# Optimization experiments

Measured on AMD Instinct MI355X. Metric: run time of the kernel, lower is better.

Reference implementation:

```python
import jax, jax.numpy as jnp
import numpy as np

DIM = 2048; H = 16; DK = 128; DV = 128; SEQ = 2048; KCONV = 4
KEY_DIM = H * DK; VAL_DIM = H * DV
EPS_L2 = 1e-6; EPS_RMS = 1e-6; SP_THRESH = 20.0


def setup_inputs() -> dict:
    key = jax.random.key(0)
    ks = jax.random.split(key, 20)
    f = jnp.float32
    def w(k, shape, scale):
        return jax.random.normal(k, shape, f) * scale
    s_in = DIM ** -0.5
    return {
        "x": jax.random.normal(ks[0], (1, SEQ, DIM), f),
        "ve": jax.random.normal(ks[1], (1, SEQ, H, DV), f),
        "sa_lambdas": jnp.array([0.7, 0.3], f),
        "Wq": w(ks[2], (DIM, KEY_DIM), s_in),
        "Wk": w(ks[3], (DIM, KEY_DIM), s_in),
        "Wv": w(ks[4], (DIM, VAL_DIM), s_in),
        "conv_q": w(ks[5], (KEY_DIM, KCONV), 0.5),
        "conv_k": w(ks[6], (KEY_DIM, KCONV), 0.5),
        "conv_v": w(ks[7], (VAL_DIM, KCONV), 0.5),
        "Wf1": w(ks[8], (DIM, DV), s_in),
        "Wf2": w(ks[9], (DV, KEY_DIM), DV ** -0.5),
        "Wb": w(ks[10], (DIM, H), s_in),
        "A_log": jnp.log(jax.random.uniform(ks[11], (H,), f, 1.0, 16.0)),
        "dt_bias": jnp.zeros((KEY_DIM,), f),
        "Wg1": w(ks[12], (DIM, DV), s_in),
        "Wg2": w(ks[13], (DV, VAL_DIM), DV ** -0.5),
        "bg2": jnp.zeros((VAL_DIM,), f),
        "norm_w": jnp.ones((DV,), f),
        "Wo": w(ks[14], (VAL_DIM, DIM), VAL_DIM ** -0.5),
    }


def _short_conv_silu(u, w):
    # u: [b, s, c], w: [c, K]; causal depthwise conv + silu
    s = u.shape[1]
    up = jnp.pad(u, ((0, 0), (w.shape[1] - 1, 0), (0, 0)))
    y = sum(up[:, i:i + s, :] * w[:, i] for i in range(w.shape[1]))
    return jax.nn.silu(y)


def _l2norm(t):
    return t * jax.lax.rsqrt(jnp.sum(t * t, axis=-1, keepdims=True) + EPS_L2)


def _forward(x, ve, sa_lambdas, Wq, Wk, Wv, conv_q, conv_k, conv_v,
             Wf1, Wf2, Wb, A_log, dt_bias, Wg1, Wg2, bg2, norm_w, Wo):
    b, s, _ = x.shape  # b == 1
    q = _short_conv_silu(x @ Wq, conv_q).reshape(b, s, H, DK)
    k = _short_conv_silu(x @ Wk, conv_k).reshape(b, s, H, DK)
    v = _short_conv_silu(x @ Wv, conv_v).reshape(b, s, H, DV)
    v = sa_lambdas[0] * v + sa_lambdas[1] * ve
    # KDA gate: per-(head, key-dim) log decay
    g = ((x @ Wf1) @ Wf2).reshape(b, s, H, DK) + dt_bias.reshape(H, DK)
    sp = jnp.where(g > SP_THRESH, g, jnp.log1p(jnp.exp(jnp.minimum(g, SP_THRESH))))
    glog = -jnp.exp(A_log)[None, None, :, None] * sp  # [b,s,h,dk]
    beta = jax.nn.sigmoid(x @ Wb)  # [b,s,h]
    # l2-normalize q,k; scale q by dk^-0.5 (chunk_kda default scale)
    qn = _l2norm(q) * (DK ** -0.5)
    kn = _l2norm(k)
    # gated delta-rule recurrence over time (b==1, squeeze batch)
    def step(S, inp):
        qt, kt, vt, gt, bt = inp  # [h,dk],[h,dk],[h,dv],[h,dk],[h]
        S = S * jnp.exp(gt)[..., None]  # per-key-channel decay
        pred = jnp.einsum('hk,hkv->hv', kt, S)
        vt_new = bt[:, None] * (vt - pred)
        S = S + kt[:, :, None] * vt_new[:, None, :]
        ot = jnp.einsum('hk,hkv->hv', qt, S)
        return S, ot
    S0 = jnp.zeros((H, DK, DV), x.dtype)
    _, o = jax.lax.scan(step, S0, (qn[0], kn[0], v[0], glog[0], beta[0]))
    o = o[None]  # [1,s,h,dv]
    # sigmoid-gated RMSNorm over head_v_dim
    gate = ((x @ Wg1) @ Wg2 + bg2).reshape(b, s, H, DV)
    var = jnp.mean(o * o, axis=-1, keepdims=True)
    o = o * jax.lax.rsqrt(var + EPS_RMS) * norm_w
    o = o * jax.nn.sigmoid(gate)
    return o.reshape(b, s, VAL_DIM) @ Wo  # [1,s,dim]


def reference(x, ve, sa_lambdas, Wq, Wk, Wv, conv_q, conv_k, conv_v,
              Wf1, Wf2, Wb, A_log, dt_bias, Wg1, Wg2, bg2, norm_w, Wo):
    return _forward(x, ve, sa_lambdas, Wq, Wk, Wv, conv_q, conv_k, conv_v,
                    Wf1, Wf2, Wb, A_log, dt_bias, Wg1, Wg2, bg2, norm_w, Wo)
```

## Files before the change

kernel.cpp:

```cpp
#include <hip/hip_runtime.h>
#include <hip/hip_bf16.h>
#include <stdint.h>
#include <stddef.h>

#define SEQL 2048
#define DIMSZ 2048
#define HN 16
#define DKD 128
#define DVD 128
#define QSCALE 0.08838834764831843f

typedef __attribute__((ext_vector_type(4))) float f32x4;
typedef __attribute__((ext_vector_type(2))) float f32x2;
typedef __attribute__((ext_vector_type(8))) short bf16x8;

__device__ __forceinline__ float sigmoid_f(float x) { return 1.f / (1.f + __expf(-x)); }
__device__ __forceinline__ float bf2f(short s) {
  union { float f; unsigned int u; } t; t.u = ((unsigned int)(unsigned short)s) << 16; return t.f;
}

#define BM 128
#define BN 128
#define BKK 64

__global__ __launch_bounds__(256) void gemm_bt(
    const __hip_bfloat16* __restrict__ A, const __hip_bfloat16* __restrict__ B,
    float* __restrict__ C, int M, int N, int lda, int ldb, int klen, int accum)
{
  __shared__ __hip_bfloat16 As[BM * BKK];
  __shared__ __hip_bfloat16 Bs[BN * BKK];
  const int tid = threadIdx.x;
  const int lane = tid & 63;
  const int w = tid >> 6;
  const int wm = w >> 1, wn = w & 1;
  const int m0 = blockIdx.y * BM, n0 = blockIdx.x * BN;
  const int l15 = lane & 15, l4 = lane >> 4;
  const int kbase = blockIdx.z * klen;

  f32x4 acc[4][4] = {};

  for (int k0 = kbase; k0 < kbase + klen; k0 += BKK) {
#pragma unroll
    for (int i = 0; i < 4; ++i) {
      const int c = (w * 4 + i) * 64 + lane;
      const int row = c >> 3;
      const int colb = (c & 7) * 8;
      __builtin_amdgcn_global_load_lds(
          (const __attribute__((address_space(1))) void*)(A + (size_t)(m0 + row) * lda + k0 + colb),
          (__attribute__((address_space(3))) void*)(As + (size_t)c * 8), 16, 0, 0);
      __builtin_amdgcn_global_load_lds(
          (const __attribute__((address_space(1))) void*)(B + (size_t)(n0 + row) * ldb + k0 + colb),
          (__attribute__((address_space(3))) void*)(Bs + (size_t)c * 8), 16, 0, 0);
    }
    __syncthreads();
#pragma unroll
    for (int kk = 0; kk < BKK; kk += 32) {
      bf16x8 af[4], bfv[4];
#pragma unroll
      for (int mi = 0; mi < 4; ++mi)
        af[mi] = *(const bf16x8*)(As + (wm * 64 + mi * 16 + l15) * BKK + kk + l4 * 8);
#pragma unroll
      for (int ni = 0; ni < 4; ++ni)
        bfv[ni] = *(const bf16x8*)(Bs + (wn * 64 + ni * 16 + l15) * BKK + kk + l4 * 8);
#pragma unroll
      for (int mi = 0; mi < 4; ++mi)
#pragma unroll
        for (int ni = 0; ni < 4; ++ni)
          acc[mi][ni] = __builtin_amdgcn_mfma_f32_16x16x32_bf16(af[mi], bfv[ni], acc[mi][ni], 0, 0, 0);
    }
    __syncthreads();
  }

  float* Cz = C + (size_t)blockIdx.z * M * N;
#pragma unroll
  for (int mi = 0; mi < 4; ++mi) {
#pragma unroll
    for (int ni = 0; ni < 4; ++ni) {
      const int row = m0 + wm * 64 + mi * 16 + l4 * 4;
      const int col = n0 + wn * 64 + ni * 16 + l15;
#pragma unroll
      for (int r = 0; r < 4; ++r) {
        size_t idx = (size_t)(row + r) * N + col;
        if (accum) Cz[idx] += acc[mi][ni][r];
        else Cz[idx] = acc[mi][ni][r];
      }
    }
  }
}

#define PHASE256(MQ, NQ, NEEDA, NEEDB)                                          \
  {                                                                             \
    if (NEEDA) {                                                                \
      _Pragma("unroll") for (int m2 = 0; m2 < 4; ++m2)                          \
      _Pragma("unroll") for (int ks = 0; ks < 2; ++ks) {                        \
        const int la = (MQ) * 128 + wm * 64 + m2 * 16 + l15;                    \
        const int kc = ks * 4 + l4;                                             \
        a[m2][ks] = *(const bf16x8*)(lds + cb + la * 64 + (kc ^ (la & 7)) * 8); \
      }                                                                         \
    }                                                                           \
    if (NEEDB) {                                                                \
      _Pragma("unroll") for (int n2 = 0; n2 < 2; ++n2)                          \
      _Pragma("unroll") for (int ks = 0; ks < 2; ++ks) {                        \
        const int lb = (NQ) * 128 + wn * 32 + n2 * 16 + l15;                    \
        const int kc = ks * 4 + l4;                                             \
        b[n2][ks] = *(const bf16x8*)(lds + cb + 16384 + lb * 64 + (kc ^ (lb & 7)) * 8); \
      }                                                                         \
    }                                                                           \
    __builtin_amdgcn_s_setprio(1);                                              \
    _Pragma("unroll") for (int m2 = 0; m2 < 4; ++m2)                            \
    _Pragma("unroll") for (int n2 = 0; n2 < 2; ++n2)                            \
    _Pragma("unroll") for (int ks = 0; ks < 2; ++ks)                            \
      acc[(MQ) * 4 + m2][(NQ) * 2 + n2] = __builtin_amdgcn_mfma_f32_16x16x32_bf16( \
          a[m2][ks], b[n2][ks], acc[(MQ) * 4 + m2][(NQ) * 2 + n2], 0, 0, 0);    \
    __builtin_amdgcn_s_setprio(0);                                              \
  }

__global__ __launch_bounds__(512, 2) void gemm_bt256(
    const __hip_bfloat16* __restrict__ A, const __hip_bfloat16* __restrict__ B,
    float* __restrict__ C, __hip_bfloat16* __restrict__ Cb,
    int M, int N, int lda, int ldb, int NT)
{
  __shared__ __hip_bfloat16 lds[65536];
  const int tid = threadIdx.x;
  const int w = tid >> 6, lane = tid & 63;
  const int wm = w >> 2, wn = w & 3;
  const int l15 = lane & 15, l4 = lane >> 4;
  const int m0 = blockIdx.y * 256, n0 = blockIdx.x * 256;

  f32x4 acc[8][4] = {};
  bf16x8 a[4][2], b[2][2];

  auto stage_half = [&](int which, int t1) {
    const int buf = t1 & 1;
    const int k0n = ((t1 < NT) ? t1 : 0) * 64;
    const int mat = which & 1;
    const int half = which >> 1;
#pragma unroll
    for (int i = 0; i < 2; ++i) {
      const int c = i * 512 + tid;
      const int l = half * 128 + (c >> 3);
      const int kcs = (c & 7) ^ (l & 7);
      const __hip_bfloat16* src;
      if (mat == 0) {
        const int grow = ((l >> 6) & 1) * 128 + (l >> 7) * 64 + (l & 63);
        src = A + (size_t)(m0 + grow) * lda + k0n + kcs * 8;
      } else {
        const int gcol = ((l >> 5) & 3) * 64 + (l >> 7) * 32 + (l & 31);
        src = B + (size_t)(n0 + gcol) * ldb + k0n + kcs * 8;
      }
      __builtin_amdgcn_global_load_lds(
          (const __attribute__((address_space(1))) void*)src,
          (__attribute__((address_space(3))) void*)(lds + (size_t)buf * 32768 + mat * 16384 + half * 8192 + (size_t)c * 8),
          16, 0, 0);
    }
  };

  stage_half(0, 0); stage_half(1, 0); stage_half(2, 0); stage_half(3, 0);

  for (int t = 0; t < NT; ++t) {
    const size_t cb = (size_t)(t & 1) * 32768;
    stage_half(0, t + 1);
    asm volatile("s_waitcnt vmcnt(6)" ::: "memory");
    __builtin_amdgcn_s_barrier();
    __builtin_amdgcn_sched_barrier(0);
    PHASE256(0, 0, 1, 1)
    __builtin_amdgcn_s_barrier();
    stage_half(1, t + 1);
    asm volatile("s_waitcnt vmcnt(4)" ::: "memory");
    __builtin_amdgcn_s_barrier();
    __builtin_amdgcn_sched_barrier(0);
    PHASE256(0, 1, 0, 1)
    __builtin_amdgcn_s_barrier();
    stage_half(2, t + 1);
    __builtin_amdgcn_s_barrier();
    __builtin_amdgcn_sched_barrier(0);
    PHASE256(1, 1, 1, 0)
    __builtin_amdgcn_s_barrier();
    stage_half(3, t + 1);
    __builtin_amdgcn_s_barrier();
    __builtin_amdgcn_sched_barrier(0);
    PHASE256(1, 0, 0, 1)
    __builtin_amdgcn_s_barrier();
  }
  asm volatile("s_waitcnt vmcnt(0)" ::: "memory");

  if (Cb) {
#pragma unroll
    for (int mi = 0; mi < 8; ++mi)
#pragma unroll
      for (int ni = 0; ni < 4; ++ni) {
        const int row = m0 + wm * 128 + mi * 16 + l4 * 4;
        const int col = n0 + wn * 64 + ni * 16 + l15;
#pragma unroll
        for (int r = 0; r < 4; ++r)
          Cb[(size_t)(row + r) * N + col] = __float2bfloat16(acc[mi][ni][r]);
      }
  } else {
#pragma unroll
    for (int mi = 0; mi < 8; ++mi)
#pragma unroll
      for (int ni = 0; ni < 4; ++ni) {
        const int row = m0 + wm * 128 + mi * 16 + l4 * 4;
        const int col = n0 + wn * 64 + ni * 16 + l15;
#pragma unroll
        for (int r = 0; r < 4; ++r)
          C[(size_t)(row + r) * N + col] = acc[mi][ni][r];
      }
  }
}

__global__ __launch_bounds__(256) void gemm_btsplit(
    const __hip_bfloat16* __restrict__ Ah, const __hip_bfloat16* __restrict__ Al,
    const __hip_bfloat16* __restrict__ Bh, const __hip_bfloat16* __restrict__ Bl,
    float* __restrict__ C, int M, int N, int lda, int ldb, int klen)
{
  __shared__ __hip_bfloat16 Ash[BM * BKK];
  __shared__ __hip_bfloat16 Asl[BM * BKK];
  __shared__ __hip_bfloat16 Bsh[BN * BKK];
  __shared__ __hip_bfloat16 Bsl[BN * BKK];
  const int tid = threadIdx.x;
  const int lane = tid & 63;
  const int w = tid >> 6;
  const int wm = w >> 1, wn = w & 1;
  const int m0 = blockIdx.y * BM, n0 = blockIdx.x * BN;
  const int l15 = lane & 15, l4 = lane >> 4;
  const int kbase = blockIdx.z * klen;

  f32x4 acc[4][4] = {};

  for (int k0 = kbase; k0 < kbase + klen; k0 += BKK) {
#pragma unroll
    for (int i = 0; i < 4; ++i) {
      const int c = (w * 4 + i) * 64 + lane;
      const int row = c >> 3;
      const int colb = (c & 7) * 8;
      const size_t go = (size_t)(m0 + row) * lda + k0 + colb;
      const size_t gn = (size_t)(n0 + row) * ldb + k0 + colb;
      __builtin_amdgcn_global_load_lds(
          (const __attribute__((address_space(1))) void*)(Ah + go),
          (__attribute__((address_space(3))) void*)(Ash + (size_t)c * 8), 16, 0, 0);
      __builtin_amdgcn_global_load_lds(
          (const __attribute__((address_space(1))) void*)(Al + go),
          (__attribute__((address_space(3))) void*)(Asl + (size_t)c * 8), 16, 0, 0);
      __builtin_amdgcn_global_load_lds(
          (const __attribute__((address_space(1))) void*)(Bh + gn),
          (__attribute__((address_space(3))) void*)(Bsh + (size_t)c * 8), 16, 0, 0);
      __builtin_amdgcn_global_load_lds(
          (const __attribute__((address_space(1))) void*)(Bl + gn),
          (__attribute__((address_space(3))) void*)(Bsl + (size_t)c * 8), 16, 0, 0);
    }
    __syncthreads();
#pragma unroll
    for (int kk = 0; kk < BKK; kk += 32) {
      bf16x8 afh[4], afl[4], bfh[4], bfl[4];
#pragma unroll
      for (int mi = 0; mi < 4; ++mi) {
        const int ao = (wm * 64 + mi * 16 + l15) * BKK + kk + l4 * 8;
        afh[mi] = *(const bf16x8*)(Ash + ao);
        afl[mi] = *(const bf16x8*)(Asl + ao);
      }
#pragma unroll
      for (int ni = 0; ni < 4; ++ni) {
        const int bo = (wn * 64 + ni * 16 + l15) * BKK + kk + l4 * 8;
        bfh[ni] = *(const bf16x8*)(Bsh + bo);
        bfl[ni] = *(const bf16x8*)(Bsl + bo);
      }
#pragma unroll
      for (int mi = 0; mi < 4; ++mi)
#pragma unroll
        for (int ni = 0; ni < 4; ++ni) {
          acc[mi][ni] = __builtin_amdgcn_mfma_f32_16x16x32_bf16(afh[mi], bfh[ni], acc[mi][ni], 0, 0, 0);
          acc[mi][ni] = __builtin_amdgcn_mfma_f32_16x16x32_bf16(afh[mi], bfl[ni], acc[mi][ni], 0, 0, 0);
          acc[mi][ni] = __builtin_amdgcn_mfma_f32_16x16x32_bf16(afl[mi], bfh[ni], acc[mi][ni], 0, 0, 0);
        }
    }
    __syncthreads();
  }

  float* Cz = C + (size_t)blockIdx.z * M * N;
#pragma unroll
  for (int mi = 0; mi < 4; ++mi) {
#pragma unroll
    for (int ni = 0; ni < 4; ++ni) {
      const int row = m0 + wm * 64 + mi * 16 + l4 * 4;
      const int col = n0 + wn * 64 + ni * 16 + l15;
#pragma unroll
      for (int r = 0; r < 4; ++r)
        Cz[(size_t)(row + r) * N + col] = acc[mi][ni][r];
    }
  }
}

__global__ __launch_bounds__(256) void transpose4_kernel(
    const float* __restrict__ Wq, const float* __restrict__ Wk,
    const float* __restrict__ Wv, const float* __restrict__ Wo,
    __hip_bfloat16* __restrict__ WqkvT, __hip_bfloat16* __restrict__ WoT)
{
  __shared__ float tile[32][33];
  const int z = blockIdx.z;
  const float* in = (z == 0) ? Wq : (z == 1) ? Wk : (z == 2) ? Wv : Wo;
  __hip_bfloat16* outT = (z < 3) ? (WqkvT + (size_t)z * 2048 * 2048) : WoT;
  const int c0 = blockIdx.x * 32, r0 = blockIdx.y * 32;
  const int tc = threadIdx.x & 31, tr = threadIdx.x >> 5;
#pragma unroll
  for (int i = 0; i < 4; ++i)
    tile[tr + i * 8][tc] = in[(size_t)(r0 + tr + i * 8) * 2048 + c0 + tc];
  __syncthreads();
#pragma unroll
  for (int i = 0; i < 4; ++i)
    outT[(size_t)(c0 + tr + i * 8) * 2048 + r0 + tc] = __float2bfloat16(tile[tc][tr + i * 8]);
}

__global__ __launch_bounds__(256) void transpose_fg1_kernel(
    const float* __restrict__ Wf1, const float* __restrict__ Wg1,
    __hip_bfloat16* __restrict__ hT, __hip_bfloat16* __restrict__ lT)
{
  __shared__ float tile[32][33];
  const int z = blockIdx.z;
  const float* in = z ? Wg1 : Wf1;
  const size_t base = (size_t)z * 128 * 2048;
  const int c0 = blockIdx.x * 32, r0 = blockIdx.y * 32;
  const int tc = threadIdx.x & 31, tr = threadIdx.x >> 5;
#pragma unroll
  for (int i = 0; i < 4; ++i)
    tile[tr + i * 8][tc] = in[(size_t)(r0 + tr + i * 8) * 128 + c0 + tc];
  __syncthreads();
#pragma unroll
  for (int i = 0; i < 4; ++i) {
    float val = tile[tc][tr + i * 8];
    __hip_bfloat16 h = __float2bfloat16(val);
    size_t oi = base + (size_t)(c0 + tr + i * 8) * 2048 + r0 + tc;
    hT[oi] = h;
    lT[oi] = z ? __float2bfloat16(0.f) : __float2bfloat16(val - __bfloat162float(h));
  }
}

__global__ __launch_bounds__(256) void transpose_f2g2_kernel(
    const float* __restrict__ Wf2, const float* __restrict__ Wg2,
    __hip_bfloat16* __restrict__ f2h, __hip_bfloat16* __restrict__ f2l,
    __hip_bfloat16* __restrict__ g2h)
{
  __shared__ float tile[32][33];
  const int z = blockIdx.z;
  const float* in = z ? Wg2 : Wf2;
  const int c0 = blockIdx.x * 32, r0 = blockIdx.y * 32;
  const int tc = threadIdx.x & 31, tr = threadIdx.x >> 5;
#pragma unroll
  for (int i = 0; i < 4; ++i)
    tile[tr + i * 8][tc] = in[(size_t)(r0 + tr + i * 8) * 2048 + c0 + tc];
  __syncthreads();
#pragma unroll
  for (int i = 0; i < 4; ++i) {
    float val = tile[tc][tr + i * 8];
    __hip_bfloat16 h = __float2bfloat16(val);
    size_t oi = (size_t)(c0 + tr + i * 8) * 128 + r0 + tc;
    if (z == 0) { f2h[oi] = h; f2l[oi] = __float2bfloat16(val - __bfloat162float(h)); }
    else g2h[oi] = h;
  }
}

__global__ __launch_bounds__(256) void cast_split_kernel(
    const float* __restrict__ in, __hip_bfloat16* __restrict__ hi,
    __hip_bfloat16* __restrict__ lo, int n4)
{
  int idx = blockIdx.x * 256 + threadIdx.x;
  if (idx >= n4) return;
  f32x4 v = *(const f32x4*)(in + (size_t)idx * 4);
  union { __hip_bfloat16 b[4]; unsigned long long u; } ph, pl;
#pragma unroll
  for (int j = 0; j < 4; ++j) {
    float f = v[j];
    __hip_bfloat16 hh = __float2bfloat16(f);
    ph.b[j] = hh;
    pl.b[j] = __float2bfloat16(f - __bfloat162float(hh));
  }
  *(unsigned long long*)((char*)hi + (size_t)idx * 8) = ph.u;
  if (lo) *(unsigned long long*)((char*)lo + (size_t)idx * 8) = pl.u;
}

__global__ __launch_bounds__(256) void reduce8_kernel(
    const float* __restrict__ part, __hip_bfloat16* __restrict__ hi,
    __hip_bfloat16* __restrict__ lo, int n4, size_t chunk)
{
  int idx = blockIdx.x * 256 + threadIdx.x;
  if (idx >= n4) return;
  f32x4 a = *(const f32x4*)(part + (size_t)idx * 4);
#pragma unroll
  for (int z = 1; z < 8; ++z) {
    f32x4 b = *(const f32x4*)(part + z * chunk + (size_t)idx * 4);
    a.x += b.x; a.y += b.y; a.z += b.z; a.w += b.w;
  }
  union { __hip_bfloat16 b[4]; unsigned long long u; } ph, pl;
#pragma unroll
  for (int j = 0; j < 4; ++j) {
    float f = a[j];
    __hip_bfloat16 hh = __float2bfloat16(f);
    ph.b[j] = hh;
    pl.b[j] = __float2bfloat16(f - __bfloat162float(hh));
  }
  *(unsigned long long*)((char*)hi + (size_t)idx * 8) = ph.u;
  if (lo) *(unsigned long long*)((char*)lo + (size_t)idx * 8) = pl.u;
}

__global__ __launch_bounds__(256) void beta_kernel(
    const float* __restrict__ x, const float* __restrict__ Wb, float* __restrict__ betaT)
{
  int idx = blockIdx.x * 256 + threadIdx.x;
  int s = idx >> 4, h = idx & 15;
  const float* xr = x + (size_t)s * DIMSZ;
  float acc = 0.f;
  for (int d = 0; d < DIMSZ; d += 4) {
    f32x4 xv = *(const f32x4*)(xr + d);
    acc = fmaf(xv.x, Wb[(size_t)(d + 0) * HN + h], acc);
    acc = fmaf(xv.y, Wb[(size_t)(d + 1) * HN + h], acc);
    acc = fmaf(xv.z, Wb[(size_t)(d + 2) * HN + h], acc);
    acc = fmaf(xv.w, Wb[(size_t)(d + 3) * HN + h], acc);
  }
  betaT[(size_t)h * SEQL + s] = 1.f / (1.f + expf(-acc));
}

#define SL20(r, d) ((r) * 160 + ((d) >> 4) * 20 + ((d) & 15))

__global__ __launch_bounds__(256) void kda_pref(
    const __hip_bfloat16* __restrict__ qkv, const float* __restrict__ ve,
    const float* __restrict__ lam,
    const float* __restrict__ cwq, const float* __restrict__ cwk, const float* __restrict__ cwv,
    const float* __restrict__ gbuf,
    const float* __restrict__ dtb, const float* __restrict__ A_log,
    const float* __restrict__ betaT,
    __hip_bfloat16* __restrict__ Xgh, __hip_bfloat16* __restrict__ KTh,
    float* __restrict__ uvS, float* __restrict__ olocS, float* __restrict__ Pg)
{
  __shared__ float GL2[32 * 160];
  __shared__ float kL2[32 * 160];
  __shared__ float qL2[32 * 132];
  __shared__ float vL2[32 * 128];
  __shared__ float ALB[32][33];
  __shared__ float Bdiag[32], betaL[32];
  __shared__ float csumW[4 * 128];

  const int bid = blockIdx.x;
  const int h = bid >> 6, cc = bid & 63;
  const int tid = threadIdx.x;
  const int w = tid >> 6, lane = tid & 63;
  const size_t hc = (size_t)h * 64 + cc;
  const float Aexp = __expf(A_log[h]);

  {
    const int c = lane * 2;
    const int r0g = cc * 32 + w * 8;
    const int cg = h * 128 + c;

    f32x4 wq0 = *(const f32x4*)(cwq + (size_t)cg * 4), wq1 = *(const f32x4*)(cwq + (size_t)(cg + 1) * 4);
    f32x4 wk0 = *(const f32x4*)(cwk + (size_t)cg * 4), wk1 = *(const f32x4*)(cwk + (size_t)(cg + 1) * 4);
    f32x4 wv0 = *(const f32x4*)(cwv + (size_t)cg * 4), wv1 = *(const f32x4*)(cwv + (size_t)(cg + 1) * 4);
    f32x2 dt2 = *(const f32x2*)(dtb + cg);
    const float l0 = lam[0], l1 = lam[1];

    f32x2 xqr[11], xkr[11], xvr[11];
#pragma unroll
    for (int i = 0; i < 11; ++i) {
      const int sr = r0g - 3 + i;
      if (sr >= 0) {
        const size_t ro = (size_t)sr * 6144 + cg;
        unsigned int uq = *(const unsigned int*)(qkv + ro);
        unsigned int uk = *(const unsigned int*)(qkv + 2048 + ro);
        unsigned int uv2 = *(const unsigned int*)(qkv + 4096 + ro);
        xqr[i].x = bf2f((short)uq);   xqr[i].y = bf2f((short)(uq >> 16));
        xkr[i].x = bf2f((short)uk);   xkr[i].y = bf2f((short)(uk >> 16));
        xvr[i].x = bf2f((short)uv2);  xvr[i].y = bf2f((short)(uv2 >> 16));
      } else {
        xqr[i].x = xqr[i].y = xkr[i].x = xkr[i].y = xvr[i].x = xvr[i].y = 0.f;
      }
    }

    float gl0[8], gl1[8];
#pragma unroll
    for (int i = 0; i < 8; ++i) {
      const int rr = r0g + i;
      const int lr = w * 8 + i;
      float aq0 = 0, aq1 = 0, ak0 = 0, ak1 = 0, av0 = 0, av1 = 0;
#pragma unroll
      for (int j = 0; j < 4; ++j) {
        aq0 = fmaf(xqr[i + j].x, wq0[j], aq0); aq1 = fmaf(xqr[i + j].y, wq1[j], aq1);
        ak0 = fmaf(xkr[i + j].x, wk0[j], ak0); ak1 = fmaf(xkr[i + j].y, wk1[j], ak1);
        av0 = fmaf(xvr[i + j].x, wv0[j], av0); av1 = fmaf(xvr[i + j].y, wv1[j], av1);
      }
      float yq0 = aq0 * sigmoid_f(aq0), yq1 = aq1 * sigmoid_f(aq1);
      float yk0 = ak0 * sigmoid_f(ak0), yk1 = ak1 * sigmoid_f(ak1);
      float yv0 = av0 * sigmoid_f(av0), yv1 = av1 * sigmoid_f(av1);

      f32x2 vev = *(const f32x2*)(ve + ((size_t)rr * HN + h) * 128 + c);
      float v0 = l0 * yv0 + l1 * vev.x;
      float v1 = l0 * yv1 + l1 * vev.y;

      float ssq = yq0 * yq0 + yq1 * yq1;
      float ssk = yk0 * yk0 + yk1 * yk1;
#pragma unroll
      for (int off = 32; off > 0; off >>= 1) {
        ssq += __shfl_xor(ssq, off);
        ssk += __shfl_xor(ssk, off);
      }
      float rq = rsqrtf(ssq + 1e-6f) * QSCALE;
      float rk = rsqrtf(ssk + 1e-6f);

      f32x2 kk; kk.x = yk0 * rk; kk.y = yk1 * rk;
      f32x2 qq; qq.x = yq0 * rq; qq.y = yq1 * rq;
      f32x2 vv; vv.x = v0; vv.y = v1;
      *(f32x2*)&kL2[SL20(lr, c)] = kk;
      *(f32x2*)&qL2[lr * 132 + c] = qq;
      *(f32x2*)&vL2[lr * 128 + c] = vv;

      f32x2 gv = *(const f32x2*)(gbuf + (size_t)rr * 2048 + cg);
      float g0 = gv.x + dt2.x, g1 = gv.y + dt2.y;
      float sp0 = (g0 > 20.f) ? g0 : log1pf(__expf(fminf(g0, 20.f)));
      float sp1 = (g1 > 20.f) ? g1 : log1pf(__expf(fminf(g1, 20.f)));
      gl0[i] = -Aexp * sp0;
      gl1[i] = -Aexp * sp1;
    }
    {
      float r0 = 0.f, r1 = 0.f;
#pragma unroll
      for (int i = 0; i < 8; ++i) { r0 += gl0[i]; gl0[i] = r0; r1 += gl1[i]; gl1[i] = r1; }
      csumW[w * 128 + c] = r0;
      csumW[w * 128 + c + 1] = r1;
    }
    if (tid < 32) betaL[tid] = betaT[(size_t)h * SEQL + cc * 32 + tid];
    __syncthreads();
    {
      float p0 = 0.f, p1 = 0.f;
      for (int wp = 0; wp < w; ++wp) { p0 += csumW[wp * 128 + c]; p1 += csumW[wp * 128 + c + 1]; }
#pragma unroll
      for (int i = 0; i < 8; ++i) {
        f32x2 gg; gg.x = gl0[i] + p0; gg.y = gl1[i] + p1;
        *(f32x2*)&GL2[SL20(w * 8 + i, c)] = gg;
      }
    }
  }
  __syncthreads();

  {
    const int tg = lane >> 3, s8 = lane & 7;
    const int tt = w * 8 + tg;
    const int ds = s8 * 20;

    float Gt[16], kt[16], qt[16];
#pragma unroll
    for (int j = 0; j < 16; j += 4) {
      *(f32x4*)&Gt[j] = *(const f32x4*)&GL2[tt * 160 + ds + j];
      *(f32x4*)&kt[j] = *(const f32x4*)&kL2[tt * 160 + ds + j];
      *(f32x4*)&qt[j] = *(const f32x4*)&qL2[tt * 132 + s8 * 16 + j];
    }
    {
      float sA = 0.f, sB = 0.f;
#pragma unroll
      for (int j = 0; j < 16; ++j) { sA = fmaf(kt[j], kt[j], sA); sB = fmaf(qt[j], kt[j], sB); }
      sA += __shfl_xor(sA, 1); sA += __shfl_xor(sA, 2); sA += __shfl_xor(sA, 4);
      sB += __shfl_xor(sB, 1); sB += __shfl_xor(sB, 2); sB += __shfl_xor(sB, 4);
      if (s8 == 0) { ALB[tt][tt] = sA; Bdiag[tt] = sB; }
    }
    const int ibound = w * 8 + 7;
    for (int i = 0; i < ibound; ++i) {
      if (i < tt) {
        float sA = 0.f, sB = 0.f;
#pragma unroll
        for (int jj = 0; jj < 4; ++jj) {
          f32x4 Gi = *(const f32x4*)&GL2[i * 160 + ds + jj * 4];
          f32x4 ki = *(const f32x4*)&kL2[i * 160 + ds + jj * 4];
#pragma unroll
          for (int u = 0; u < 4; ++u) {
            float e = __expf(Gt[jj * 4 + u] - Gi[u]);
            float kid = ki[u] * e;
            sA = fmaf(kt[jj * 4 + u], kid, sA);
            sB = fmaf(qt[jj * 4 + u], kid, sB);
          }
        }
        sA += __shfl_xor(sA, 1); sA += __shfl_xor(sA, 2); sA += __shfl_xor(sA, 4);
        sB += __shfl_xor(sB, 1); sB += __shfl_xor(sB, 2); sB += __shfl_xor(sB, 4);
        if (s8 == 0) { ALB[tt][i] = sA; ALB[i][tt] = sB; }
      }
    }
  }
  __syncthreads();

  const int col = tid & 127, half = tid >> 7;
  const size_t rowbase = (size_t)(cc * 32) * 2048 + h * 128 + col;
  const int rbase = half * 16;
  {
    const float g31 = GL2[SL20(31, col)];
    size_t kb = hc * 4096 + (size_t)col * 32;
#pragma unroll
    for (int i = 0; i < 16; ++i) {
      int r = rbase + i;
      float kv = kL2[SL20(r, col)] * __expf(g31 - GL2[SL20(r, col)]);
      KTh[kb + r] = __float2bfloat16(kv);
    }
  }

  if (half == 0) {
    float expg[32];
#pragma unroll
    for (int r = 0; r < 32; ++r) expg[r] = __expf(GL2[SL20(r, col)]);

    float uvr[32], wr[32];
#pragma unroll
    for (int r = 0; r < 32; ++r) {
      float suv = 0.f, sw = 0.f;
#pragma unroll
      for (int j = 0; j < 32; ++j) {
        if (j < r) { float a = ALB[r][j]; suv = fmaf(a, uvr[j], suv); sw = fmaf(a, wr[j], sw); }
      }
      float br = betaL[r];
      float khr = kL2[SL20(r, col)] * expg[r];
      uvr[r] = br * (vL2[r * 128 + col] - suv);
      wr[r] = br * (khr - sw);
      uvS[rowbase + (size_t)r * 2048] = uvr[r];
      Xgh[hc * 8192 + (size_t)(32 + r) * 128 + col] = __float2bfloat16(wr[r]);
    }

#pragma unroll
    for (int r = 0; r < 32; ++r) {
      float qtv = qL2[r * 132 + col] * expg[r];
      float ol = 0.f;
#pragma unroll
      for (int j = 0; j < 32; ++j) {
        if (j < r) { float b = ALB[j][r]; qtv = fmaf(-b, wr[j], qtv); ol = fmaf(b, uvr[j], ol); }
      }
      { float b = Bdiag[r]; qtv = fmaf(-b, wr[r], qtv); ol = fmaf(b, uvr[r], ol); }
      Xgh[hc * 8192 + (size_t)r * 128 + col] = __float2bfloat16(qtv);
      olocS[rowbase + (size_t)r * 2048] = ol;
    }
    Pg[hc * 128 + col] = expg[31];
  }
}

#define STP 136
#define UTP 40

struct ChunkOps {
  bf16x8 ah[4];
  bf16x8 kah[2];
  f32x4 pvv[2];
  float pB[4];
};

__global__ __launch_bounds__(256) void kda_seq(
    const __hip_bfloat16* __restrict__ Xgh, const __hip_bfloat16* __restrict__ KTh,
    const float* __restrict__ uvS, const float* __restrict__ olocS,
    const float* __restrict__ Pg, float* __restrict__ obuf)
{
  __shared__ __hip_bfloat16 STh[16 * STP], STl[16 * STP];
  __shared__ __hip_bfloat16 UTh[16 * UTP];
  const int tid = threadIdx.x;
  const int w = tid >> 6, lane = tid & 63, l15 = lane & 15, l4 = lane >> 4;
  const int h = blockIdx.x >> 3, vq = blockIdx.x & 7;
  const int v0 = vq * 16;
  const int r0 = (w & 1) * 16 + l4 * 4;
  const int isO = (w < 2);

  for (int i = tid; i < 16 * STP; i += 256) {
    STh[i] = __float2bfloat16(0.f);
    STl[i] = __float2bfloat16(0.f);
  }
  __syncthreads();

  f32x4 S[2] = {};

  auto loadops = [&](ChunkOps& o, int c) {
    const size_t hc = (size_t)h * 64 + c;
    const __hip_bfloat16* xh = Xgh + hc * 8192 + (size_t)(w * 16 + l15) * 128 + l4 * 8;
#pragma unroll
    for (int kk = 0; kk < 4; ++kk) o.ah[kk] = *(const bf16x8*)(xh + kk * 32);
    const float* pb = (isO ? olocS : uvS) + (size_t)(c * 32 + r0) * 2048 + h * 128 + v0 + l15;
#pragma unroll
    for (int r = 0; r < 4; ++r) o.pB[r] = pb[(size_t)r * 2048];
#pragma unroll
    for (int mi = 0; mi < 2; ++mi) {
      const int kd = (w * 2 + mi) * 16;
      o.kah[mi] = *(const bf16x8*)(KTh + hc * 4096 + (size_t)(kd + l15) * 32 + l4 * 8);
      o.pvv[mi] = *(const f32x4*)(Pg + hc * 128 + kd + l4 * 4);
    }
  };

  auto body = [&](ChunkOps& o, int c) {
    f32x4 Y = {};
#pragma unroll
    for (int kk = 0; kk < 4; ++kk) {
      const int so = l15 * STP + kk * 32 + l4 * 8;
      bf16x8 bh = *(const bf16x8*)(STh + so);
      bf16x8 bl = *(const bf16x8*)(STl + so);
      Y = __builtin_amdgcn_mfma_f32_16x16x32_bf16(o.ah[kk], bh, Y, 0, 0, 0);
      Y = __builtin_amdgcn_mfma_f32_16x16x32_bf16(o.ah[kk], bl, Y, 0, 0, 0);
    }

    if (isO) {
      size_t ob = (size_t)(c * 32 + r0) * 2048 + h * 128 + v0 + l15;
#pragma unroll
      for (int r = 0; r < 4; ++r)
        obuf[ob + (size_t)r * 2048] = Y[r] + o.pB[r];
    } else {
      union { __hip_bfloat16 b[4]; unsigned long long u; } uh;
#pragma unroll
      for (int r = 0; r < 4; ++r)
        uh.b[r] = __float2bfloat16(o.pB[r] - Y[r]);
      *(unsigned long long*)(UTh + l15 * UTP + r0) = uh.u;
    }
    __syncthreads();

#pragma unroll
    for (int mi = 0; mi < 2; ++mi) S[mi] *= o.pvv[mi];
    {
      bf16x8 ubh = *(const bf16x8*)(UTh + l15 * UTP + l4 * 8);
#pragma unroll
      for (int mi = 0; mi < 2; ++mi)
        S[mi] = __builtin_amdgcn_mfma_f32_16x16x32_bf16(o.kah[mi], ubh, S[mi], 0, 0, 0);
    }

#pragma unroll
    for (int mi = 0; mi < 2; ++mi) {
      const int kd0 = (w * 2 + mi) * 16 + l4 * 4;
      union { __hip_bfloat16 b[4]; unsigned long long u; } sh, sl;
#pragma unroll
      for (int r = 0; r < 4; ++r) {
        __hip_bfloat16 hh = __float2bfloat16(S[mi][r]);
        sh.b[r] = hh;
        sl.b[r] = __float2bfloat16(S[mi][r] - __bfloat162float(hh));
      }
      *(unsigned long long*)(STh + l15 * STP + kd0) = sh.u;
      *(unsigned long long*)(STl + l15 * STP + kd0) = sl.u;
    }
    __syncthreads();
  };

  ChunkOps A_, B_;
  loadops(A_, 0);
  for (int c = 0; c < 64; c += 2) {
    loadops(B_, c + 1);
    body(A_, c);
    if (c + 2 < 64) loadops(A_, c + 2);
    body(B_, c + 1);
  }
}

__global__ __launch_bounds__(256) void rmsgate_kernel(
    const float* __restrict__ o, const float* __restrict__ gate,
    const float* __restrict__ bg2, const float* __restrict__ norm_w,
    __hip_bfloat16* __restrict__ og)
{
  int row = blockIdx.x * 4 + (threadIdx.x >> 6);
  int lane = threadIdx.x & 63;
  int s = row >> 4, h = row & 15;
  int j = lane * 2;
  const float* p = o + (size_t)row * 128 + j;
  f32x2 v = *(const f32x2*)p;
  float ss = v.x * v.x + v.y * v.y;
#pragma unroll
  for (int off = 32; off > 0; off >>= 1) ss += __shfl_xor(ss, off);
  float rs = rsqrtf(ss * (1.f / 128.f) + 1e-6f);
  int c = h * 128 + j;
  float g0 = gate[(size_t)s * 2048 + c] + bg2[c];
  float g1 = gate[(size_t)s * 2048 + c + 1] + bg2[c + 1];
  float o0 = v.x * rs * norm_w[j] * (1.f / (1.f + expf(-g0)));
  float o1 = v.y * rs * norm_w[j + 1] * (1.f / (1.f + expf(-g1)));
  union { __hip_bfloat16 b[2]; unsigned int u; } pk2;
  pk2.b[0] = __float2bfloat16(o0);
  pk2.b[1] = __float2bfloat16(o1);
  *(unsigned int*)((char*)og + ((size_t)s * 2048 + c) * 2) = pk2.u;
}

extern "C" void kernel_launch(void* const* d_in, const int* in_sizes, int n_in,
                              void* d_out, int out_size, void* d_ws, size_t ws_size,
                              hipStream_t stream)
{
  const float* x      = (const float*)d_in[0];
  const float* ve     = (const float*)d_in[1];
  const float* lam    = (const float*)d_in[2];
  const float* Wq     = (const float*)d_in[3];
  const float* Wk     = (const float*)d_in[4];
  const float* Wv     = (const float*)d_in[5];
  const float* cwq    = (const float*)d_in[6];
  const float* cwk    = (const float*)d_in[7];
  const float* cwv    = (const float*)d_in[8];
  const float* Wf1    = (const float*)d_in[9];
  const float* Wf2    = (const float*)d_in[10];
  const float* Wb     = (const float*)d_in[11];
  const float* A_log  = (const float*)d_in[12];
  const float* dtb    = (const float*)d_in[13];
  const float* Wg1    = (const float*)d_in[14];
  const float* Wg2    = (const float*)d_in[15];
  const float* bg2    = (const float*)d_in[16];
  const float* norm_w = (const float*)d_in[17];
  const float* Wo     = (const float*)d_in[18];
  float* out = (float*)d_out;

  const size_t S2 = (size_t)2048 * 2048;

  char* p = (char*)d_ws;
  auto alloc = [&](size_t bytes) { char* r = p; p += (bytes + 255) & ~(size_t)255; return r; };

  __hip_bfloat16* xb     = (__hip_bfloat16*)alloc(S2 * 2);
  __hip_bfloat16* WoT    = (__hip_bfloat16*)alloc(S2 * 2);
  __hip_bfloat16* Wf2hT  = (__hip_bfloat16*)alloc(2048 * 128 * 2);
  __hip_bfloat16* Wf2lT  = (__hip_bfloat16*)alloc(2048 * 128 * 2);
  __hip_bfloat16* Wg2T   = (__hip_bfloat16*)alloc(2048 * 128 * 2);
  __hip_bfloat16* Wfg1hT = (__hip_bfloat16*)alloc((size_t)256 * 2048 * 2);
  __hip_bfloat16* Wfg1lT = (__hip_bfloat16*)alloc((size_t)256 * 2048 * 2);
  __hip_bfloat16* f1g1h  = (__hip_bfloat16*)alloc((size_t)2048 * 256 * 2);
  __hip_bfloat16* f1g1l  = (__hip_bfloat16*)alloc((size_t)2048 * 256 * 2);
  float* betaT = (float*)alloc((size_t)2048 * 16 * 4);
  __hip_bfloat16* qkvb = (__hip_bfloat16*)alloc(3 * S2 * 2);
  float* gbuf  = (float*)alloc(S2 * 4);
  float* gatebuf = (float*)alloc(S2 * 4);
  float* uvS   = (float*)alloc(S2 * 4);
  float* olocS = (float*)alloc(S2 * 4);
  __hip_bfloat16* Xgh = (__hip_bfloat16*)alloc(S2 * 4);
  __hip_bfloat16* KTh = (__hip_bfloat16*)alloc(S2 * 2);
  float* Pg    = (float*)alloc((size_t)1024 * 128 * 4);

  __hip_bfloat16* WqkvT = (__hip_bfloat16*)uvS;
  __hip_bfloat16* xlo = (__hip_bfloat16*)((char*)olocS + S2 * 2);
  float* fpart = (float*)Xgh;
  float* obuf  = gbuf;
  __hip_bfloat16* og = (__hip_bfloat16*)qkvb;

  cast_split_kernel<<<4096, 256, 0, stream>>>(x, xb, xlo, (int)(S2 / 4));

  transpose4_kernel<<<dim3(64, 64, 4), 256, 0, stream>>>(Wq, Wk, Wv, Wo, WqkvT, WoT);
  transpose_fg1_kernel<<<dim3(4, 64, 2), 256, 0, stream>>>(Wf1, Wg1, Wfg1hT, Wfg1lT);
  transpose_f2g2_kernel<<<dim3(64, 4, 2), 256, 0, stream>>>(Wf2, Wg2, Wf2hT, Wf2lT, Wg2T);

  gemm_bt256<<<dim3(24, 8), 512, 0, stream>>>(xb, WqkvT, nullptr, qkvb, 2048, 6144, 2048, 2048, 32);

  gemm_btsplit<<<dim3(2, 16, 8), 256, 0, stream>>>(xb, xlo, Wfg1hT, Wfg1lT, fpart,
                                                   2048, 256, 2048, 2048, 256);
  reduce8_kernel<<<512, 256, 0, stream>>>(fpart, f1g1h, f1g1l, 131072, (size_t)2048 * 256);

  gemm_btsplit<<<dim3(16, 16), 256, 0, stream>>>(f1g1h, f1g1l, Wf2hT, Wf2lT, gbuf,
                                                 2048, 2048, 256, 128, 128);
  gemm_bt<<<dim3(16, 16), 256, 0, stream>>>(f1g1h + 128, Wg2T, gatebuf,
                                            2048, 2048, 256, 128, 128, 0);

  beta_kernel<<<128, 256, 0, stream>>>(x, Wb, betaT);

  kda_pref<<<1024, 256, 0, stream>>>(qkvb, ve, lam, cwq, cwk, cwv, gbuf, dtb, A_log, betaT,
                                     Xgh, KTh, uvS, olocS, Pg);

  kda_seq<<<128, 256, 0, stream>>>(Xgh, KTh, uvS, olocS, Pg, obuf);

  rmsgate_kernel<<<8192, 256, 0, stream>>>(obuf, gatebuf, bg2, norm_w, og);

  gemm_bt<<<dim3(16, 16), 256, 0, stream>>>(og, WoT, out, 2048, 2048, 2048, 2048, 2048, 0);
}
```

Measured before the change: 382.4 us.

## Retile QKV projection GEMM to 256x192 blocks for full CU coverage

The QKV projection GEMM moves from 256x256 tiles (192 blocks) to 256x192 tiles (256 blocks), so the grid matches the 256 compute units of the MI355X and leaves fewer idle. The staging and phase schedule is reworked into six sub-phases, with new waitcnt values and a narrower B tile per wave. The change costs a lower MFMA-to-load ratio per tile and restricts occupancy to one block per CU via launch bounds. The fp32 output path is removed because this kernel only writes bf16.

After: 375.5 us. No clear change (-1.8%).

```diff
diff --git a/kernel.cpp b/kernel.cpp
--- a/kernel.cpp
+++ b/kernel.cpp
@@ -88,125 +88,123 @@
   }
 }
 
-#define PHASE256(MQ, NQ, NEEDA, NEEDB)                                          \
-  {                                                                             \
-    if (NEEDA) {                                                                \
-      _Pragma("unroll") for (int m2 = 0; m2 < 4; ++m2)                          \
-      _Pragma("unroll") for (int ks = 0; ks < 2; ++ks) {                        \
-        const int la = (MQ) * 128 + wm * 64 + m2 * 16 + l15;                    \
-        const int kc = ks * 4 + l4;                                             \
-        a[m2][ks] = *(const bf16x8*)(lds + cb + la * 64 + (kc ^ (la & 7)) * 8); \
-      }                                                                         \
-    }                                                                           \
-    if (NEEDB) {                                                                \
-      _Pragma("unroll") for (int n2 = 0; n2 < 2; ++n2)                          \
-      _Pragma("unroll") for (int ks = 0; ks < 2; ++ks) {                        \
-        const int lb = (NQ) * 128 + wn * 32 + n2 * 16 + l15;                    \
-        const int kc = ks * 4 + l4;                                             \
-        b[n2][ks] = *(const bf16x8*)(lds + cb + 16384 + lb * 64 + (kc ^ (lb & 7)) * 8); \
-      }                                                                         \
-    }                                                                           \
-    __builtin_amdgcn_s_setprio(1);                                              \
-    _Pragma("unroll") for (int m2 = 0; m2 < 4; ++m2)                            \
-    _Pragma("unroll") for (int n2 = 0; n2 < 2; ++n2)                            \
-    _Pragma("unroll") for (int ks = 0; ks < 2; ++ks)                            \
-      acc[(MQ) * 4 + m2][(NQ) * 2 + n2] = __builtin_amdgcn_mfma_f32_16x16x32_bf16( \
-          a[m2][ks], b[n2][ks], acc[(MQ) * 4 + m2][(NQ) * 2 + n2], 0, 0, 0);    \
-    __builtin_amdgcn_s_setprio(0);                                              \
-  }
-
-__global__ __launch_bounds__(512, 2) void gemm_bt256(
+__global__ __launch_bounds__(512, 1) void gemm_bt192(
     const __hip_bfloat16* __restrict__ A, const __hip_bfloat16* __restrict__ B,
-    float* __restrict__ C, __hip_bfloat16* __restrict__ Cb,
-    int M, int N, int lda, int ldb, int NT)
-{
-  __shared__ __hip_bfloat16 lds[65536];
+    __hip_bfloat16* __restrict__ Cb, int N, int lda, int ldb, int NT)
+{
+  __shared__ __hip_bfloat16 lds[57344];
   const int tid = threadIdx.x;
   const int w = tid >> 6, lane = tid & 63;
   const int wm = w >> 2, wn = w & 3;
   const int l15 = lane & 15, l4 = lane >> 4;
-  const int m0 = blockIdx.y * 256, n0 = blockIdx.x * 256;
-
-  f32x4 acc[8][4] = {};
-  bf16x8 a[4][2], b[2][2];
-
-  auto stage_half = [&](int which, int t1) {
+  const int m0 = blockIdx.y * 256, n0 = blockIdx.x * 192;
+
+  f32x4 acc[8][3] = {};
+  bf16x8 a[4][2], b[2];
+
+  auto stage_a = [&](int half, int t1) {
     const int buf = t1 & 1;
     const int k0n = ((t1 < NT) ? t1 : 0) * 64;
-    const int mat = which & 1;
-    const int half = which >> 1;
 #pragma unroll
     for (int i = 0; i < 2; ++i) {
       const int c = i * 512 + tid;
       const int l = half * 128 + (c >> 3);
       const int kcs = (c & 7) ^ (l & 7);
-      const __hip_bfloat16* src;
-      if (mat == 0) {
-        const int grow = ((l >> 6) & 1) * 128 + (l >> 7) * 64 + (l & 63);
-        src = A + (size_t)(m0 + grow) * lda + k0n + kcs * 8;
-      } else {
-        const int gcol = ((l >> 5) & 3) * 64 + (l >> 7) * 32 + (l & 31);
-        src = B + (size_t)(n0 + gcol) * ldb + k0n + kcs * 8;
-      }
+      const int grow = ((l >> 6) & 1) * 128 + (l >> 7) * 64 + (l & 63);
       __builtin_amdgcn_global_load_lds(
-          (const __attribute__((address_space(1))) void*)src,
-          (__attribute__((address_space(3))) void*)(lds + (size_t)buf * 32768 + mat * 16384 + half * 8192 + (size_t)c * 8),
+          (const __attribute__((address_space(1))) void*)(A + (size_t)(m0 + grow) * lda + k0n + kcs * 8),
+          (__attribute__((address_space(3))) void*)(lds + (size_t)buf * 28672 + half * 8192 + (size_t)c * 8),
           16, 0, 0);
     }
   };
-
-  stage_half(0, 0); stage_half(1, 0); stage_half(2, 0); stage_half(3, 0);
+  auto stage_b = [&](int j, int t1) {
+    const int buf = t1 & 1;
+    const int k0n = ((t1 < NT) ? t1 : 0) * 64;
+    const int c = tid;
+    const int l = j * 64 + (c >> 3);
+    const int kcs = (c & 7) ^ (l & 7);
+    __builtin_amdgcn_global_load_lds(
+        (const __attribute__((address_space(1))) void*)(B + (size_t)(n0 + l) * ldb + k0n + kcs * 8),
+        (__attribute__((address_space(3))) void*)(lds + (size_t)buf * 28672 + 16384 + j * 4096 + (size_t)c * 8),
+        16, 0, 0);
+  };
+
+  auto phase = [&](size_t cb, int MQ, int NQ, bool needA) {
+    if (needA) {
+#pragma unroll
+      for (int m2 = 0; m2 < 4; ++m2)
+#pragma unroll
+        for (int ks = 0; ks < 2; ++ks) {
+          const int la = MQ * 128 + wm * 64 + m2 * 16 + l15;
+          const int kc = ks * 4 + l4;
+          a[m2][ks] = *(const bf16x8*)(lds + cb + la * 64 + (kc ^ (la & 7)) * 8);
+        }
+    }
+#pragma unroll
+    for (int ks = 0; ks < 2; ++ks) {
+      const int lb = NQ * 64 + wn * 16 + l15;
+      const int kc = ks * 4 + l4;
+      b[ks] = *(const bf16x8*)(lds + cb + 16384 + lb * 64 + (kc ^ (lb & 7)) * 8);
+    }
+    __builtin_amdgcn_s_setprio(1);
+#pragma unroll
+    for (int m2 = 0; m2 < 4; ++m2)
+#pragma unroll
+      for (int ks = 0; ks < 2; ++ks)
+        acc[MQ * 4 + m2][NQ] = __builtin_amdgcn_mfma_f32_16x16x32_bf16(
+            a[m2][ks], b[ks], acc[MQ * 4 + m2][NQ], 0, 0, 0);
+    __builtin_amdgcn_s_setprio(0);
+  };
+
+  stage_a(0, 0); stage_a(1, 0); stage_b(0, 0); stage_b(1, 0); stage_b(2, 0);
 
   for (int t = 0; t < NT; ++t) {
-    const size_t cb = (size_t)(t & 1) * 32768;
-    stage_half(0, t + 1);
-    asm volatile("s_waitcnt vmcnt(6)" ::: "memory");
+    const size_t cb = (size_t)(t & 1) * 28672;
+    stage_a(0, t + 1);
+    asm volatile("s_waitcnt vmcnt(4)" ::: "memory");
     __builtin_amdgcn_s_barrier();
     __builtin_amdgcn_sched_barrier(0);
-    PHASE256(0, 0, 1, 1)
-    __builtin_amdgcn_s_barrier();
-    stage_half(1, t + 1);
-    asm volatile("s_waitcnt vmcnt(4)" ::: "memory");
+    phase(cb, 0, 0, true);
+    __builtin_amdgcn_s_barrier();
+    stage_a(1, t + 1);
+    asm volatile("s_waitcnt vmcnt(5)" ::: "memory");
     __builtin_amdgcn_s_barrier();
     __builtin_amdgcn_sched_barrier(0);
-    PHASE256(0, 1, 0, 1)
-    __builtin_amdgcn_s_barrier();
-    stage_half(2, t + 1);
+    phase(cb, 0, 1, false);
+    __builtin_amdgcn_s_barrier();
+    stage_b(0, t + 1);
+    asm volatile("s_waitcnt vmcnt(5)" ::: "memory");
     __builtin_amdgcn_s_barrier();
     __builtin_amdgcn_sched_barrier(0);
-    PHASE256(1, 1, 1, 0)
-    __builtin_amdgcn_s_barrier();
-    stage_half(3, t + 1);
+    phase(cb, 0, 2, false);
+    __builtin_amdgcn_s_barrier();
+    stage_b(1, t + 1);
     __builtin_amdgcn_s_barrier();
     __builtin_amdgcn_sched_barrier(0);
-    PHASE256(1, 0, 0, 1)
+    phase(cb, 1, 0, true);
+    __builtin_amdgcn_s_barrier();
+    stage_b(2, t + 1);
+    __builtin_amdgcn_s_barrier();
+    __builtin_amdgcn_sched_barrier(0);
+    phase(cb, 1, 1, false);
+    __builtin_amdgcn_s_barrier();
+    __builtin_amdgcn_s_barrier();
+    __builtin_amdgcn_sched_barrier(0);
+    phase(cb, 1, 2, false);
     __builtin_amdgcn_s_barrier();
   }
   asm volatile("s_waitcnt vmcnt(0)" ::: "memory");
 
-  if (Cb) {
-#pragma unroll
-    for (int mi = 0; mi < 8; ++mi)
-#pragma unroll
-      for (int ni = 0; ni < 4; ++ni) {
-        const int row = m0 + wm * 128 + mi * 16 + l4 * 4;
-        const int col = n0 + wn * 64 + ni * 16 + l15;
-#pragma unroll
-        for (int r = 0; r < 4; ++r)
-          Cb[(size_t)(row + r) * N + col] = __float2bfloat16(acc[mi][ni][r]);
-      }
-  } else {
-#pragma unroll
-    for (int mi = 0; mi < 8; ++mi)
-#pragma unroll
-      for (int ni = 0; ni < 4; ++ni) {
-        const int row = m0 + wm * 128 + mi * 16 + l4 * 4;
-        const int col = n0 + wn * 64 + ni * 16 + l15;
-#pragma unroll
-        for (int r = 0; r < 4; ++r)
-          C[(size_t)(row + r) * N + col] = acc[mi][ni][r];
-      }
-  }
+#pragma unroll
+  for (int mi = 0; mi < 8; ++mi)
+#pragma unroll
+    for (int nq = 0; nq < 3; ++nq) {
+      const int row = m0 + wm * 128 + mi * 16 + l4 * 4;
+      const int col = n0 + nq * 64 + wn * 16 + l15;
+#pragma unroll
+      for (int r = 0; r < 4; ++r)
+        Cb[(size_t)(row + r) * N + col] = __float2bfloat16(acc[mi][nq][r]);
+    }
 }
 
 __global__ __launch_bounds__(256) void gemm_btsplit(
@@ -829,7 +827,7 @@
   transpose_fg1_kernel<<<dim3(4, 64, 2), 256, 0, stream>>>(Wf1, Wg1, Wfg1hT, Wfg1lT);
   transpose_f2g2_kernel<<<dim3(64, 4, 2), 256, 0, stream>>>(Wf2, Wg2, Wf2hT, Wf2lT, Wg2T);
 
-  gemm_bt256<<<dim3(24, 8), 512, 0, stream>>>(xb, WqkvT, nullptr, qkvb, 2048, 6144, 2048, 2048, 32);
+  gemm_bt192<<<dim3(32, 8), 512, 0, stream>>>(xb, WqkvT, qkvb, 6144, 2048, 2048, 32);
 
   gemm_btsplit<<<dim3(2, 16, 8), 256, 0, stream>>>(xb, xlo, Wfg1hT, Wfg1lT, fpart,
                                                    2048, 256, 2048, 2048, 256);
```
